# Kernel tuning notes

Hardware: AMD Instinct MI355X
Metric: run time of the kernel (lower is better)

The kernel has to match this reference:

```python
import jax, jax.numpy as jnp
import numpy as np

NUM_NODES = 100000
NUM_EDGES = 1200000
IN_CH = 64
HID_CH = 64
NUM_REL = 8
DEG = NUM_EDGES // NUM_NODES  # uniform degree 12


def setup_inputs() -> dict:
    key = jax.random.key(0)
    k1, k2, k3, k4 = jax.random.split(key, 4)
    x = jax.random.normal(k1, (NUM_NODES, IN_CH), dtype=jnp.float32)
    linear = jax.random.normal(k2, (NUM_REL, IN_CH, HID_CH), dtype=jnp.float32) * (1.0 / np.sqrt(IN_CH))
    ptr = jnp.arange(NUM_NODES + 1, dtype=jnp.int64) * DEG  # CSR row pointers, uniform degree
    idx = jax.random.randint(k3, (NUM_EDGES,), 0, NUM_NODES, dtype=jnp.int64)
    edge_types = jax.random.randint(k4, (NUM_EDGES,), 0, NUM_REL, dtype=jnp.int64)
    return {"x": x, "linear": linear, "ptr": ptr, "idx": idx,
            "edge_types": edge_types, "num_node": NUM_NODES}


def reference(x, linear, ptr, idx, edge_types, num_node):
    # Gather source-node features per edge: [E, in]
    gathered = x[idx]
    # Per-edge-type linear transform (loop over small fixed num_rel, like RGCNOP)
    out_e = jnp.zeros((gathered.shape[0], linear.shape[-1]), dtype=gathered.dtype)
    for r in range(linear.shape[0]):
        mask = (edge_types == r).astype(gathered.dtype)[:, None]
        out_e = out_e + mask * (gathered @ linear[r])
    # CSR scatter-sum aggregation over destination segments defined by ptr
    num_edges = idx.shape[0]
    seg_ids = jnp.searchsorted(ptr, jnp.arange(num_edges, dtype=ptr.dtype), side='right') - 1
    agg = jax.ops.segment_sum(out_e, seg_ids, num_segments=num_node)
    # Degree normalization
    deg = (ptr[1:] - ptr[:-1]).astype(agg.dtype)
    return agg / deg[:, None]
```

## Files before the change

### kernel.cpp

```cpp
#include <hip/hip_runtime.h>
#include <hip/hip_bf16.h>


#define THREADS 512
#define NPB 32
#define KDIM 512
#define LDA 520
#define MAXE 512
#define WFRAG (4 * 16 * 64 * 8)

typedef __attribute__((ext_vector_type(8))) short bf16x8;
typedef __attribute__((ext_vector_type(4))) float f32x4;

extern __shared__ __align__(16) char smem[];

__device__ __forceinline__ unsigned short f2bf(float f) {
  __hip_bfloat16 h = __float2bfloat16(f);
  return *reinterpret_cast<unsigned short*>(&h);
}

__global__ __launch_bounds__(256) void pack_w(const void* __restrict__ wv,
                                              unsigned short* __restrict__ wsB) {
  const int lane = threadIdx.x & 63;
  const unsigned word = ((const unsigned*)wv)[lane];
  const int exf = (int)((word >> 7) & 0xFFu);
  const bool w_bf16 = __popcll(__ballot(exf >= 96 && exf < 160)) >= 48;
  for (int i = blockIdx.x * 256 + threadIdx.x; i < WFRAG; i += gridDim.x * 256) {
    const int j  = i & 7;
    const int l  = (i >> 3) & 63;
    const int kt = (i >> 9) & 15;
    const int nt = i >> 13;
    const int k  = kt * 32 + (l >> 4) * 8 + j;
    const int n  = nt * 16 + (l & 15);
    float v;
    if (w_bf16) v = __bfloat162float(((const __hip_bfloat16*)wv)[k * 64 + n]);
    else        v = ((const float*)wv)[k * 64 + n];
    wsB[i] = f2bf(v);
  }
}

#define ACC_SW(accrow, r, vv)                                        \
  switch (r) {                                                       \
    case 0: accrow[0] += (vv); break; case 1: accrow[1] += (vv); break; \
    case 2: accrow[2] += (vv); break; case 3: accrow[3] += (vv); break; \
    case 4: accrow[4] += (vv); break; case 5: accrow[5] += (vv); break; \
    case 6: accrow[6] += (vv); break; default: accrow[7] += (vv); break; }

__global__ __launch_bounds__(THREADS, 6)
void rgcn_fused(const void* __restrict__ xv,
                const void* __restrict__ wv,
                const int* __restrict__ p32,
                const int* __restrict__ i32,
                const int* __restrict__ t32,
                const unsigned short* __restrict__ wsB,
                float* __restrict__ out,
                int num_nodes) {
  __hip_bfloat16* aggS = (__hip_bfloat16*)smem;
  __hip_bfloat16* wtS  = aggS + NPB * LDA;
  char* tail = smem + (size_t)NPB * LDA * 2 + (wsB ? 0 : (size_t)64 * LDA * 2);
  float*    invS  = (float*)tail;
  int*      ptrS  = (int*)(tail + 256);
  unsigned* eMeta = (unsigned*)(tail + 256 + 144);

  const int tid   = threadIdx.x;
  const int lane  = tid & 63;
  const int wvid  = tid >> 6;
  const int node0 = blockIdx.x * NPB;

  const unsigned xword = ((const unsigned*)xv)[lane];
  const int exf = (int)((xword >> 7) & 0xFFu);
  const bool x_bf16 = __popcll(__ballot(exf >= 96 && exf < 160)) >= 48;
  const bool idx64 = (p32[1] == 0);

  auto ldptr = [&](int n) -> int { return idx64 ? p32[2 * n] : p32[n]; };

  const int ntop   = min(node0 + NPB, num_nodes);
  const int e_lo   = ldptr(node0);
  const int ecount = ldptr(ntop) - e_lo;
  const bool staged = (ecount > 0 && ecount <= MAXE);

  for (int i = tid; i <= NPB; i += THREADS)
    ptrS[i] = ldptr(min(node0 + i, num_nodes));

  if (staged) {
    for (int e = tid; e < ecount; e += THREADS) {
      const int ge = e_lo + e;
      const unsigned s = (unsigned)(idx64 ? i32[2 * ge] : i32[ge]);
      const unsigned r = (unsigned)(idx64 ? t32[2 * ge] : t32[ge]);
      eMeta[e] = s | (r << 24);
    }
  }

  if (!wsB) {
    if (x_bf16) {
      const __hip_bfloat16* wb = (const __hip_bfloat16*)wv;
      for (int i = tid; i < KDIM * 64; i += THREADS)
        wtS[(i & 63) * LDA + (i >> 6)] = wb[i];
    } else {
      const float* wf = (const float*)wv;
      for (int i = tid; i < KDIM * 64; i += THREADS)
        wtS[(i & 63) * LDA + (i >> 6)] = __float2bfloat16(wf[i]);
    }
  }

  __syncthreads();

  for (int i = tid; i < NPB; i += THREADS) {
    const int d = ptrS[i + 1] - ptrS[i];
    invS[i] = (d > 0 && node0 + i < num_nodes) ? 1.0f / (float)d : 0.0f;
  }

  const int c16 = lane & 15;
  const int qd  = lane >> 4;

  auto gather = [&](auto xp, auto loadrow) {
    const int nlb = wvid * 4;
    const int eq0 = ptrS[nlb + qd] - e_lo;
    const int dq  = ptrS[nlb + qd + 1] - e_lo - eq0;
    const bool okfast = staged && (node0 + nlb + 3 < num_nodes) &&
                        (__ballot(dq == 12) == ~0ull);
    if (okfast) {
      f32x4 acc[8];
#pragma unroll
      for (int r = 0; r < 8; ++r) acc[r] = (f32x4){0.f, 0.f, 0.f, 0.f};
#pragma unroll
      for (int h = 0; h < 2; ++h) {
        unsigned mB[6];
#pragma unroll
        for (int j = 0; j < 6; ++j) mB[j] = eMeta[eq0 + h * 6 + j];
        f32x4 v[6];
#pragma unroll
        for (int j = 0; j < 6; ++j)
          v[j] = loadrow((int)(mB[j] & 0x00FFFFFFu), c16);
#pragma unroll
        for (int j = 0; j < 6; ++j) {
          const unsigned rj = mB[j] >> 24;
#pragma unroll
          for (int r = 0; r < 8; ++r) {
            const float mk = (rj == (unsigned)r) ? 1.0f : 0.0f;
            const f32x4 m4 = {mk, mk, mk, mk};
            acc[r] += m4 * v[j];
          }
        }
      }
      unsigned short* dst = (unsigned short*)(aggS + (nlb + qd) * LDA) + 4 * c16;
#pragma unroll
      for (int r = 0; r < 8; ++r) {
        ushort4 b;
        b.x = f2bf(acc[r][0]); b.y = f2bf(acc[r][1]);
        b.z = f2bf(acc[r][2]); b.w = f2bf(acc[r][3]);
        *(ushort4*)(dst + r * 64) = b;
      }
    } else {
#pragma unroll
      for (int t = 0; t < 4; ++t) {
        const int nl = nlb + t;
        float a[8] = {0.f, 0.f, 0.f, 0.f, 0.f, 0.f, 0.f, 0.f};
        if (node0 + nl < num_nodes) {
          const int e0 = ptrS[nl] - e_lo, e1 = ptrS[nl + 1] - e_lo;
          for (int e = e0; e < e1; ++e) {
            unsigned mm;
            if (staged) mm = eMeta[e];
            else {
              const int ge = e_lo + e;
              mm = (unsigned)(idx64 ? i32[2 * ge] : i32[ge]) |
                   ((unsigned)(idx64 ? t32[2 * ge] : t32[ge]) << 24);
            }
            const float vv = (float)xp[(size_t)(mm & 0x00FFFFFFu) * 64 + lane];
            const int r = __builtin_amdgcn_readfirstlane((int)(mm >> 24));
            ACC_SW(a, r, vv)
          }
        }
#pragma unroll
        for (int r = 0; r < 8; ++r)
          aggS[nl * LDA + r * 64 + lane] = __float2bfloat16(a[r]);
      }
    }
  };

  if (x_bf16) {
    const __hip_bfloat16* xb = (const __hip_bfloat16*)xv;
    auto lr = [&](int src, int c) -> f32x4 {
      const ushort4 u = ((const ushort4*)xv)[(size_t)src * 16 + c];
      f32x4 f;
      f[0] = __uint_as_float((unsigned)(unsigned short)u.x << 16);
      f[1] = __uint_as_float((unsigned)(unsigned short)u.y << 16);
      f[2] = __uint_as_float((unsigned)(unsigned short)u.z << 16);
      f[3] = __uint_as_float((unsigned)(unsigned short)u.w << 16);
      return f;
    };
    gather(xb, lr);
  } else {
    const float* xf = (const float*)xv;
    auto lr = [&](int src, int c) -> f32x4 {
      return ((const f32x4*)xv)[(size_t)src * 16 + c];
    };
    gather(xf, lr);
  }

  __syncthreads();

  const int mt = wvid >> 2;
  const int nt = wvid & 3;
  const int mi = lane & 15;
  const int q4 = lane >> 4;
  const __hip_bfloat16* ap = aggS + (mt * 16 + mi) * LDA + q4 * 8;
  f32x4 c0 = {0.f, 0.f, 0.f, 0.f};
  if (wsB) {
    const bf16x8* B = (const bf16x8*)wsB;
#pragma unroll
    for (int kt = 0; kt < KDIM / 32; ++kt) {
      const bf16x8 a = *(const bf16x8*)(ap + kt * 32);
      const bf16x8 b = B[(nt * 16 + kt) * 64 + lane];
      c0 = __builtin_amdgcn_mfma_f32_16x16x32_bf16(a, b, c0, 0, 0, 0);
    }
  } else {
    const __hip_bfloat16* bp = wtS + (nt * 16 + mi) * LDA + q4 * 8;
#pragma unroll
    for (int kt = 0; kt < KDIM / 32; ++kt) {
      const bf16x8 a = *(const bf16x8*)(ap + kt * 32);
      const bf16x8 b = *(const bf16x8*)(bp + kt * 32);
      c0 = __builtin_amdgcn_mfma_f32_16x16x32_bf16(a, b, c0, 0, 0, 0);
    }
  }

#pragma unroll
  for (int i = 0; i < 4; ++i) {
    const int row  = q4 * 4 + i;
    const int nl   = mt * 16 + row;
    const int node = node0 + nl;
    if (node < num_nodes) {
      out[(size_t)node * 64 + nt * 16 + mi] = c0[i] * invS[nl];
    }
  }
}

extern "C" void kernel_launch(void* const* d_in, const int* in_sizes, int n_in,
                              void* d_out, int out_size, void* d_ws, size_t ws_size,
                              hipStream_t stream) {
  const void* x   = d_in[0];
  const void* w   = d_in[1];
  const int*  ptr = (const int*)d_in[2];
  const int*  idx = (const int*)d_in[3];
  const int*  et  = (const int*)d_in[4];
  float*      out = (float*)d_out;

  const int num_nodes = in_sizes[0] / 64;

  const bool useWs = (d_ws != nullptr) &&
                     (ws_size >= (size_t)WFRAG * sizeof(unsigned short));
  unsigned short* wsB = useWs ? (unsigned short*)d_ws : nullptr;
  if (useWs) pack_w<<<32, 256, 0, stream>>>(w, wsB);

  const size_t lds_bytes = (size_t)NPB * LDA * 2 +
                           (useWs ? 0 : (size_t)64 * LDA * 2) +
                           256 + 144 + (size_t)MAXE * 4;

  hipFuncSetAttribute((const void*)rgcn_fused,
                      hipFuncAttributeMaxDynamicSharedMemorySize,
                      (int)lds_bytes);

  const int nblocks = (num_nodes + NPB - 1) / NPB;
  rgcn_fused<<<nblocks, THREADS, lds_bytes, stream>>>(x, w, ptr, idx, et, wsB,
                                                      out, num_nodes);
}
```

Baseline: 134.3 us.

## Accumulate per-relation sums with fp32 LDS atomics instead of masked registers

The fast gather path drops the 8-way masked register accumulation and instead adds each gathered row into an fp32 LDS buffer indexed by edge type using atomicAdd. The buffer is zeroed first and converted to bf16 in place before the MFMA stage. The aim is to remove the 8x masked FMA work and register pressure, at the cost of doubled LDS footprint, extra zeroing and conversion passes, extra barriers, and LDS atomic contention. Occupancy hint is lowered from 6 to 4 blocks.

```diff
diff --git a/kernel.cpp b/kernel.cpp
--- a/kernel.cpp
+++ b/kernel.cpp
@@ -11,6 +11,7 @@
 
 typedef __attribute__((ext_vector_type(8))) short bf16x8;
 typedef __attribute__((ext_vector_type(4))) float f32x4;
+typedef __attribute__((ext_vector_type(8))) unsigned short u16x8;
 
 extern __shared__ __align__(16) char smem[];
 
@@ -46,7 +47,7 @@
     case 4: accrow[4] += (vv); break; case 5: accrow[5] += (vv); break; \
     case 6: accrow[6] += (vv); break; default: accrow[7] += (vv); break; }
 
-__global__ __launch_bounds__(THREADS, 6)
+__global__ __launch_bounds__(THREADS, 4)
 void rgcn_fused(const void* __restrict__ xv,
                 const void* __restrict__ wv,
                 const int* __restrict__ p32,
@@ -55,9 +56,10 @@
                 const unsigned short* __restrict__ wsB,
                 float* __restrict__ out,
                 int num_nodes) {
+  float*          aggF = (float*)smem;
   __hip_bfloat16* aggS = (__hip_bfloat16*)smem;
-  __hip_bfloat16* wtS  = aggS + NPB * LDA;
-  char* tail = smem + (size_t)NPB * LDA * 2 + (wsB ? 0 : (size_t)64 * LDA * 2);
+  __hip_bfloat16* wtS  = (__hip_bfloat16*)(smem + (size_t)NPB * LDA * 4);
+  char* tail = smem + (size_t)NPB * LDA * 4 + (wsB ? 0 : (size_t)64 * LDA * 2);
   float*    invS  = (float*)tail;
   int*      ptrS  = (int*)(tail + 256);
   unsigned* eMeta = (unsigned*)(tail + 256 + 144);
@@ -89,6 +91,12 @@
       const unsigned r = (unsigned)(idx64 ? t32[2 * ge] : t32[ge]);
       eMeta[e] = s | (r << 24);
     }
+  }
+
+  {
+    f32x4* z = (f32x4*)aggF;
+    const f32x4 zero = {0.f, 0.f, 0.f, 0.f};
+    for (int i = tid; i < NPB * LDA / 4; i += THREADS) z[i] = zero;
   }
 
   if (!wsB) {
@@ -120,36 +128,21 @@
     const bool okfast = staged && (node0 + nlb + 3 < num_nodes) &&
                         (__ballot(dq == 12) == ~0ull);
     if (okfast) {
-      f32x4 acc[8];
-#pragma unroll
-      for (int r = 0; r < 8; ++r) acc[r] = (f32x4){0.f, 0.f, 0.f, 0.f};
-#pragma unroll
-      for (int h = 0; h < 2; ++h) {
-        unsigned mB[6];
-#pragma unroll
-        for (int j = 0; j < 6; ++j) mB[j] = eMeta[eq0 + h * 6 + j];
-        f32x4 v[6];
-#pragma unroll
-        for (int j = 0; j < 6; ++j)
-          v[j] = loadrow((int)(mB[j] & 0x00FFFFFFu), c16);
-#pragma unroll
-        for (int j = 0; j < 6; ++j) {
-          const unsigned rj = mB[j] >> 24;
-#pragma unroll
-          for (int r = 0; r < 8; ++r) {
-            const float mk = (rj == (unsigned)r) ? 1.0f : 0.0f;
-            const f32x4 m4 = {mk, mk, mk, mk};
-            acc[r] += m4 * v[j];
-          }
-        }
-      }
-      unsigned short* dst = (unsigned short*)(aggS + (nlb + qd) * LDA) + 4 * c16;
-#pragma unroll
-      for (int r = 0; r < 8; ++r) {
-        ushort4 b;
-        b.x = f2bf(acc[r][0]); b.y = f2bf(acc[r][1]);
-        b.z = f2bf(acc[r][2]); b.w = f2bf(acc[r][3]);
-        *(ushort4*)(dst + r * 64) = b;
+      unsigned m[12];
+#pragma unroll
+      for (int j = 0; j < 12; ++j) m[j] = eMeta[eq0 + j];
+      f32x4 v[12];
+#pragma unroll
+      for (int j = 0; j < 12; ++j)
+        v[j] = loadrow((int)(m[j] & 0x00FFFFFFu), c16);
+      float* qbase = aggF + (size_t)(nlb + qd) * LDA + c16 * 4;
+#pragma unroll
+      for (int j = 0; j < 12; ++j) {
+        float* dst = qbase + ((m[j] >> 24) << 6);
+        atomicAdd(dst + 0, v[j][0]);
+        atomicAdd(dst + 1, v[j][1]);
+        atomicAdd(dst + 2, v[j][2]);
+        atomicAdd(dst + 3, v[j][3]);
       }
     } else {
 #pragma unroll
@@ -173,7 +166,7 @@
         }
 #pragma unroll
         for (int r = 0; r < 8; ++r)
-          aggS[nl * LDA + r * 64 + lane] = __float2bfloat16(a[r]);
+          aggF[(size_t)nl * LDA + r * 64 + lane] = a[r];
       }
     }
   };
@@ -200,11 +193,38 @@
 
   __syncthreads();
 
+  {
+    const int row = tid >> 4;
+    const int cb  = (tid & 15) * 32;
+    const int rp  = tid & 3;
+    f32x4 uA[4], uB[4];
+#pragma unroll
+    for (int k = 0; k < 4; ++k) {
+      const int p = (k + rp) & 3;
+      const float* src = aggF + (size_t)row * LDA + cb + p * 8;
+      uA[k] = *(const f32x4*)(src);
+      uB[k] = *(const f32x4*)(src + 4);
+    }
+    __syncthreads();
+#pragma unroll
+    for (int k = 0; k < 4; ++k) {
+      const int p = (k + rp) & 3;
+      u16x8 w;
+      w[0] = f2bf(uA[k][0]); w[1] = f2bf(uA[k][1]);
+      w[2] = f2bf(uA[k][2]); w[3] = f2bf(uA[k][3]);
+      w[4] = f2bf(uB[k][0]); w[5] = f2bf(uB[k][1]);
+      w[6] = f2bf(uB[k][2]); w[7] = f2bf(uB[k][3]);
+      *(u16x8*)(aggS + (size_t)row * LDA + cb + p * 8) = w;
+    }
+  }
+
+  __syncthreads();
+
   const int mt = wvid >> 2;
   const int nt = wvid & 3;
   const int mi = lane & 15;
   const int q4 = lane >> 4;
-  const __hip_bfloat16* ap = aggS + (mt * 16 + mi) * LDA + q4 * 8;
+  const __hip_bfloat16* ap = aggS + (size_t)(mt * 16 + mi) * LDA + q4 * 8;
   f32x4 c0 = {0.f, 0.f, 0.f, 0.f};
   if (wsB) {
     const bf16x8* B = (const bf16x8*)wsB;
@@ -215,7 +235,7 @@
       c0 = __builtin_amdgcn_mfma_f32_16x16x32_bf16(a, b, c0, 0, 0, 0);
     }
   } else {
-    const __hip_bfloat16* bp = wtS + (nt * 16 + mi) * LDA + q4 * 8;
+    const __hip_bfloat16* bp = wtS + (size_t)(nt * 16 + mi) * LDA + q4 * 8;
 #pragma unroll
     for (int kt = 0; kt < KDIM / 32; ++kt) {
       const bf16x8 a = *(const bf16x8*)(ap + kt * 32);
@@ -252,7 +272,7 @@
   unsigned short* wsB = useWs ? (unsigned short*)d_ws : nullptr;
   if (useWs) pack_w<<<32, 256, 0, stream>>>(w, wsB);
 
-  const size_t lds_bytes = (size_t)NPB * LDA * 2 +
+  const size_t lds_bytes = (size_t)NPB * LDA * 4 +
                            (useWs ? 0 : (size_t)64 * LDA * 2) +
                            256 + 144 + (size_t)MAXE * 4;
 
```

Result: slower. 516.9 us (+285.0%).

## Sort edges by relation per node and segment-sum gathered rows with run-end stores

Applied to the files above, without the earlier changes.

Each node's 12 edges are counting-sorted by relation type in LDS so that, in the fast path, a wave accumulates consecutive same-type rows and writes one bf16 partial per relation run. Non-final elements of a run go to a dummy LDS row, which keeps the stores branch-free. This replaces the 8-way masked FMA accumulation per edge with one vector add per edge. It adds a per-node sort pass, zeroing of the aggregation buffer, an extra sync and one extra LDS row, and it increases LDS stores and register pressure because all 12 rows are loaded at once.

```diff
diff --git a/kernel.cpp b/kernel.cpp
--- a/kernel.cpp
+++ b/kernel.cpp
@@ -56,8 +56,9 @@
                 float* __restrict__ out,
                 int num_nodes) {
   __hip_bfloat16* aggS = (__hip_bfloat16*)smem;
-  __hip_bfloat16* wtS  = aggS + NPB * LDA;
-  char* tail = smem + (size_t)NPB * LDA * 2 + (wsB ? 0 : (size_t)64 * LDA * 2);
+  __hip_bfloat16* wtS  = aggS + (NPB + 1) * LDA;
+  char* tail = smem + (size_t)(NPB + 1) * LDA * 2 +
+               (wsB ? 0 : (size_t)64 * LDA * 2);
   float*    invS  = (float*)tail;
   int*      ptrS  = (int*)(tail + 256);
   unsigned* eMeta = (unsigned*)(tail + 256 + 144);
@@ -110,6 +111,45 @@
     invS[i] = (d > 0 && node0 + i < num_nodes) ? 1.0f / (float)d : 0.0f;
   }
 
+  if (staged) {
+    for (int n = tid; n < NPB; n += THREADS) {
+      const int b0 = ptrS[n] - e_lo;
+      const int d  = ptrS[n + 1] - ptrS[n];
+      if (d == 12) {
+        unsigned mm[12];
+        unsigned long long cnt = 0;
+#pragma unroll
+        for (int i = 0; i < 12; ++i) {
+          mm[i] = eMeta[b0 + i];
+          cnt += 1ull << ((mm[i] >> 24) * 4);
+        }
+        unsigned long long off = 0;
+        unsigned run = 0;
+#pragma unroll
+        for (int r = 0; r < 8; ++r) {
+          off |= (unsigned long long)run << (r * 4);
+          run += (unsigned)((cnt >> (r * 4)) & 15ull);
+        }
+#pragma unroll
+        for (int i = 0; i < 12; ++i) {
+          const int sh = (int)(mm[i] >> 24) * 4;
+          const unsigned slot = (unsigned)((off >> sh) & 15ull);
+          off += 1ull << sh;
+          eMeta[b0 + (int)slot] = mm[i];
+        }
+      }
+    }
+  }
+
+  {
+    f32x4* z = (f32x4*)aggS;
+    const f32x4 zero = {0.f, 0.f, 0.f, 0.f};
+    const int nvec = (NPB + 1) * LDA * 2 / 16;
+    for (int i = tid; i < nvec; i += THREADS) z[i] = zero;
+  }
+
+  __syncthreads();
+
   const int c16 = lane & 15;
   const int qd  = lane >> 4;
 
@@ -120,36 +160,31 @@
     const bool okfast = staged && (node0 + nlb + 3 < num_nodes) &&
                         (__ballot(dq == 12) == ~0ull);
     if (okfast) {
-      f32x4 acc[8];
-#pragma unroll
-      for (int r = 0; r < 8; ++r) acc[r] = (f32x4){0.f, 0.f, 0.f, 0.f};
-#pragma unroll
-      for (int h = 0; h < 2; ++h) {
-        unsigned mB[6];
-#pragma unroll
-        for (int j = 0; j < 6; ++j) mB[j] = eMeta[eq0 + h * 6 + j];
-        f32x4 v[6];
-#pragma unroll
-        for (int j = 0; j < 6; ++j)
-          v[j] = loadrow((int)(mB[j] & 0x00FFFFFFu), c16);
-#pragma unroll
-        for (int j = 0; j < 6; ++j) {
-          const unsigned rj = mB[j] >> 24;
-#pragma unroll
-          for (int r = 0; r < 8; ++r) {
-            const float mk = (rj == (unsigned)r) ? 1.0f : 0.0f;
-            const f32x4 m4 = {mk, mk, mk, mk};
-            acc[r] += m4 * v[j];
-          }
-        }
-      }
-      unsigned short* dst = (unsigned short*)(aggS + (nlb + qd) * LDA) + 4 * c16;
-#pragma unroll
-      for (int r = 0; r < 8; ++r) {
-        ushort4 b;
-        b.x = f2bf(acc[r][0]); b.y = f2bf(acc[r][1]);
-        b.z = f2bf(acc[r][2]); b.w = f2bf(acc[r][3]);
-        *(ushort4*)(dst + r * 64) = b;
+      unsigned m[12];
+      unsigned rr[12];
+#pragma unroll
+      for (int j = 0; j < 12; ++j) m[j] = eMeta[eq0 + j];
+#pragma unroll
+      for (int j = 0; j < 12; ++j) rr[j] = m[j] >> 24;
+      f32x4 v[12];
+#pragma unroll
+      for (int j = 0; j < 12; ++j)
+        v[j] = loadrow((int)(m[j] & 0x00FFFFFFu), c16);
+      unsigned short* nodeP =
+          (unsigned short*)(aggS + (size_t)(nlb + qd) * LDA) + 4 * c16;
+      unsigned short* dumpP =
+          (unsigned short*)(aggS + (size_t)NPB * LDA) + qd * 136 + 4 * c16;
+      f32x4 A = {0.f, 0.f, 0.f, 0.f};
+#pragma unroll
+      for (int j = 0; j < 12; ++j) {
+        A += v[j];
+        const bool b = (j == 11) || (rr[j] != rr[j + 1 < 12 ? j + 1 : 11]);
+        ushort4 bb;
+        bb.x = f2bf(A[0]); bb.y = f2bf(A[1]);
+        bb.z = f2bf(A[2]); bb.w = f2bf(A[3]);
+        unsigned short* dst = b ? (nodeP + (rr[j] << 6)) : dumpP;
+        *(ushort4*)dst = bb;
+        A = b ? (f32x4){0.f, 0.f, 0.f, 0.f} : A;
       }
     } else {
 #pragma unroll
@@ -173,7 +208,7 @@
         }
 #pragma unroll
         for (int r = 0; r < 8; ++r)
-          aggS[nl * LDA + r * 64 + lane] = __float2bfloat16(a[r]);
+          aggS[(size_t)nl * LDA + r * 64 + lane] = __float2bfloat16(a[r]);
       }
     }
   };
@@ -204,7 +239,7 @@
   const int nt = wvid & 3;
   const int mi = lane & 15;
   const int q4 = lane >> 4;
-  const __hip_bfloat16* ap = aggS + (mt * 16 + mi) * LDA + q4 * 8;
+  const __hip_bfloat16* ap = aggS + (size_t)(mt * 16 + mi) * LDA + q4 * 8;
   f32x4 c0 = {0.f, 0.f, 0.f, 0.f};
   if (wsB) {
     const bf16x8* B = (const bf16x8*)wsB;
@@ -215,7 +250,7 @@
       c0 = __builtin_amdgcn_mfma_f32_16x16x32_bf16(a, b, c0, 0, 0, 0);
     }
   } else {
-    const __hip_bfloat16* bp = wtS + (nt * 16 + mi) * LDA + q4 * 8;
+    const __hip_bfloat16* bp = wtS + (size_t)(nt * 16 + mi) * LDA + q4 * 8;
 #pragma unroll
     for (int kt = 0; kt < KDIM / 32; ++kt) {
       const bf16x8 a = *(const bf16x8*)(ap + kt * 32);
@@ -252,7 +287,7 @@
   unsigned short* wsB = useWs ? (unsigned short*)d_ws : nullptr;
   if (useWs) pack_w<<<32, 256, 0, stream>>>(w, wsB);
 
-  const size_t lds_bytes = (size_t)NPB * LDA * 2 +
+  const size_t lds_bytes = (size_t)(NPB + 1) * LDA * 2 +
                            (useWs ? 0 : (size_t)64 * LDA * 2) +
                            256 + 144 + (size_t)MAXE * 4;
 
```

Measured after the change: 131.9 us. About the same (-1.7%).
